# Kernel tuning notes

Measured on AMD Instinct MI355X. Metric: run time of the kernel, lower is better.

## Reference

```python
import jax, jax.numpy as jnp
import numpy as np

B, N, D, H = 4, 2048, 256, 8
d = D // H          # 32 per-head dim
EPS = 1e-5
SCALE = 1.0 / float(np.sqrt(d))


def setup_inputs() -> dict:
    key = jax.random.key(0)
    ks = jax.random.split(key, 6)
    s = 0.02
    x = jax.random.normal(ks[0], (B, N, D), jnp.float32)
    # RoPE frequencies: theta_j = 10000^(-2j/d), angle = pos * theta
    inv_freq = 1.0 / (10000.0 ** (jnp.arange(0, d, 2, dtype=jnp.float32) / d))  # (d/2,)
    ang = jnp.arange(N, dtype=jnp.float32)[:, None] * inv_freq[None, :]          # (N, d/2)
    return {
        "x": x,
        "freqs_cos": jnp.cos(ang),
        "freqs_sin": jnp.sin(ang),
        "w_qkv": jax.random.normal(ks[1], (D, 3 * D), jnp.float32) * s,
        "b_qkv": jnp.zeros((3 * D,), jnp.float32),
        "w_proj": jax.random.normal(ks[2], (D, D), jnp.float32) * s,
        "b_proj": jnp.zeros((D,), jnp.float32),
        "ln1_g": jnp.ones((D,), jnp.float32),
        "ln1_b": jnp.zeros((D,), jnp.float32),
        "ln2_g": jnp.ones((D,), jnp.float32),
        "ln2_b": jnp.zeros((D,), jnp.float32),
        "w1": jax.random.normal(ks[3], (D, 2 * D), jnp.float32) * s,
        "b1": jnp.zeros((2 * D,), jnp.float32),
        "w2": jax.random.normal(ks[4], (2 * D, D), jnp.float32) * s,
        "b2": jnp.zeros((D,), jnp.float32),
    }


def _layer_norm(x, g, b):
    mu = jnp.mean(x, axis=-1, keepdims=True)
    var = jnp.mean(jnp.square(x - mu), axis=-1, keepdims=True)
    return (x - mu) * jax.lax.rsqrt(var + EPS) * g + b


def _rope(t, cos, sin):
    # t: (B,H,N,d); interleaved (even,odd) pairs viewed as complex, multiplied by e^{i*ang}
    tr = t.reshape(B, H, N, d // 2, 2)
    te, to = tr[..., 0], tr[..., 1]
    c = cos[None, None, :, :]
    s = sin[None, None, :, :]
    oe = te * c - to * s
    oo = te * s + to * c
    return jnp.stack([oe, oo], axis=-1).reshape(B, H, N, d)


def reference(x, freqs_cos, freqs_sin, w_qkv, b_qkv, w_proj, b_proj,
              ln1_g, ln1_b, ln2_g, ln2_b, w1, b1, w2, b2):
    # Pre-LN MHSA with RoPE (dropout = identity at eval)
    h = _layer_norm(x, ln1_g, ln1_b)
    qkv = (h @ w_qkv + b_qkv).reshape(B, N, 3, H, d).transpose(0, 2, 3, 1, 4)  # (B,3,H,N,d)
    q, k, v = qkv[:, 0], qkv[:, 1], qkv[:, 2]
    q = _rope(q, freqs_cos, freqs_sin)
    k = _rope(k, freqs_cos, freqs_sin)
    attn = jax.nn.softmax(jnp.einsum('bhnd,bhmd->bhnm', q, k) * SCALE, axis=-1)
    out = jnp.einsum('bhnm,bhmd->bhnd', attn, v).transpose(0, 2, 1, 3).reshape(B, N, D)
    x = x + (out @ w_proj + b_proj)
    h = _layer_norm(x, ln2_g, ln2_b)
    ffn = jax.nn.relu(h @ w1 + b1) @ w2 + b2
    return x + ffn
```

## Files before the change

### kernel.cpp

```cpp
#include <hip/hip_runtime.h>
#include <hip/hip_bf16.h>
#include <math.h>

#define Bsz 4
#define Nseq 2048
#define Dm 256
#define Hh 8
#define Hd 32
#define EPS_ 1e-5f
#define SCALE_ 0.17677669529663687f

typedef __attribute__((ext_vector_type(8))) short short8;
typedef __attribute__((ext_vector_type(4))) short short4v;
typedef __attribute__((ext_vector_type(4))) float f32x4;

__device__ __forceinline__ void gload16(const void* g, void* l) {
    __builtin_amdgcn_global_load_lds(
        (const __attribute__((address_space(1))) void*)g,
        (__attribute__((address_space(3))) void*)l, 16, 0, 0);
}

__device__ __forceinline__ short8 read8x2(const __hip_bfloat16* p) {
    short4v lo = *(const short4v*)p;
    short4v hi = *(const short4v*)(p + 4);
    return __builtin_shufflevector(lo, hi, 0, 1, 2, 3, 4, 5, 6, 7);
}

__global__ __launch_bounds__(256) void ln_kernel(const float* __restrict__ x,
                                                 const float* __restrict__ g,
                                                 const float* __restrict__ b,
                                                 __hip_bfloat16* __restrict__ out) {
    int row  = blockIdx.x * 4 + (threadIdx.x >> 6);
    int lane = threadIdx.x & 63;
    const float* xr = x + (size_t)row * Dm;
    float4 v = *(const float4*)(xr + lane * 4);
    float s  = v.x + v.y + v.z + v.w;
    float ss = v.x * v.x + v.y * v.y + v.z * v.z + v.w * v.w;
    #pragma unroll
    for (int off = 32; off; off >>= 1) {
        s  += __shfl_xor(s, off);
        ss += __shfl_xor(ss, off);
    }
    float mu  = s * (1.0f / Dm);
    float var = ss * (1.0f / Dm) - mu * mu;
    float rs  = rsqrtf(var + EPS_);
    float4 gv = *(const float4*)(g + lane * 4);
    float4 bv = *(const float4*)(b + lane * 4);
    float o0 = (v.x - mu) * rs * gv.x + bv.x;
    float o1 = (v.y - mu) * rs * gv.y + bv.y;
    float o2 = (v.z - mu) * rs * gv.z + bv.z;
    float o3 = (v.w - mu) * rs * gv.w + bv.w;
    __hip_bfloat16 h0 = __float2bfloat16(o0), h1 = __float2bfloat16(o1);
    __hip_bfloat16 h2 = __float2bfloat16(o2), h3 = __float2bfloat16(o3);
    short4v o4 = { *(short*)&h0, *(short*)&h1, *(short*)&h2, *(short*)&h3 };
    *(short4v*)(out + (size_t)row * Dm + lane * 4) = o4;
}

__global__ __launch_bounds__(256) void wconv_kernel(
    const float* __restrict__ s0, const float* __restrict__ s1,
    const float* __restrict__ s2, const float* __restrict__ s3,
    __hip_bfloat16* __restrict__ d0, __hip_bfloat16* __restrict__ d1,
    __hip_bfloat16* __restrict__ d2, __hip_bfloat16* __restrict__ d3) {
    __shared__ float t[32][33];
    int bid = blockIdx.x;
    const float* src; __hip_bfloat16* dst; int K, N, tb;
    if (bid < 192)      { src = s0; dst = d0; K = 256; N = 768; tb = bid; }
    else if (bid < 256) { src = s1; dst = d1; K = 256; N = 256; tb = bid - 192; }
    else if (bid < 384) { src = s2; dst = d2; K = 256; N = 512; tb = bid - 256; }
    else                { src = s3; dst = d3; K = 512; N = 256; tb = bid - 384; }
    int tn = N >> 5;
    int k0 = (tb / tn) * 32, n0 = (tb % tn) * 32;
    int c = threadIdx.x & 31, r0 = threadIdx.x >> 5;
    #pragma unroll
    for (int i = 0; i < 4; i++) {
        int r = r0 + i * 8;
        t[r][c] = src[(size_t)(k0 + r) * N + n0 + c];
    }
    __syncthreads();
    #pragma unroll
    for (int i = 0; i < 4; i++) {
        int n = r0 + i * 8;
        dst[(size_t)(n0 + n) * K + k0 + c] = __float2bfloat16(t[c][n]);
    }
}

template <int EPI>
__global__ __launch_bounds__(256) void mfma_gemm(const __hip_bfloat16* __restrict__ A,
                                                 const __hip_bfloat16* __restrict__ Wt,
                                                 const float* __restrict__ bias,
                                                 const float* __restrict__ res,
                                                 float* __restrict__ Cf,
                                                 __hip_bfloat16* __restrict__ Cb,
                                                 int M, int Nn, int K) {
    __shared__ __align__(16) __hip_bfloat16 As[128 * 32];
    __shared__ __align__(16) __hip_bfloat16 Bs[64 * 32];
    const int tid = threadIdx.x, w = tid >> 6, lane = tid & 63;
    const int lm = lane & 15, lq = lane >> 4;
    const int bm = blockIdx.y * 128, bn = blockIdx.x * 64;
    f32x4 acc[2][4];
    #pragma unroll
    for (int i = 0; i < 2; i++)
        #pragma unroll
        for (int j = 0; j < 4; j++) acc[i][j] = (f32x4){0.f, 0.f, 0.f, 0.f};

    const int sw = (lq ^ (lm & 3)) * 8;
    for (int k0 = 0; k0 < K; k0 += 32) {
        #pragma unroll
        for (int p = 0; p < 2; p++) {
            int c = p * 256 + w * 64 + lane;
            int r = c >> 2, gk = ((c & 3) ^ (r & 3)) * 8;
            gload16(A + (size_t)(bm + r) * K + k0 + gk, As + (p * 256 + w * 64) * 8);
        }
        {
            int c = w * 64 + lane;
            int r = c >> 2, gk = ((c & 3) ^ (r & 3)) * 8;
            gload16(Wt + (size_t)(bn + r) * K + k0 + gk, Bs + (w * 64) * 8);
        }
        __syncthreads();
        short8 a0 = *(const short8*)&As[(w * 32 + lm) * 32 + sw];
        short8 a1 = *(const short8*)&As[(w * 32 + 16 + lm) * 32 + sw];
        #pragma unroll
        for (int nf = 0; nf < 4; nf++) {
            short8 bfr = *(const short8*)&Bs[(nf * 16 + lm) * 32 + sw];
            acc[0][nf] = __builtin_amdgcn_mfma_f32_16x16x32_bf16(a0, bfr, acc[0][nf], 0, 0, 0);
            acc[1][nf] = __builtin_amdgcn_mfma_f32_16x16x32_bf16(a1, bfr, acc[1][nf], 0, 0, 0);
        }
        __syncthreads();
    }
    #pragma unroll
    for (int nf = 0; nf < 4; nf++) {
        int cg = bn + nf * 16 + lm;
        float bi = bias[cg];
        #pragma unroll
        for (int mf = 0; mf < 2; mf++) {
            #pragma unroll
            for (int r = 0; r < 4; r++) {
                int rg = bm + w * 32 + mf * 16 + lq * 4 + r;
                float v = acc[mf][nf][r] + bi;
                if (EPI == 1) {
                    v = fmaxf(v, 0.f);
                    Cb[(size_t)rg * Nn + cg] = __float2bfloat16(v);
                } else {
                    v += res[(size_t)rg * Nn + cg];
                    Cf[(size_t)rg * Nn + cg] = v;
                }
            }
        }
    }
}

__global__ __launch_bounds__(256) void qkv_mfma(const __hip_bfloat16* __restrict__ A,
                                                const __hip_bfloat16* __restrict__ Wt,
                                                const float* __restrict__ bias,
                                                const float* __restrict__ fcos,
                                                const float* __restrict__ fsin,
                                                __hip_bfloat16* __restrict__ qout,
                                                __hip_bfloat16* __restrict__ kout,
                                                __hip_bfloat16* __restrict__ vout) {
    const int K = 256, Nn = 768;
    __shared__ __align__(16) __hip_bfloat16 As[128 * 32];
    __shared__ __align__(16) __hip_bfloat16 Bs[64 * 32];
    __shared__ __align__(16) float cosS[2048];
    __shared__ __align__(16) float sinS[2048];
    const int tid = threadIdx.x, w = tid >> 6, lane = tid & 63;
    const int lm = lane & 15, lq = lane >> 4;
    const int bm = blockIdx.y * 128, bn = blockIdx.x * 64;
    f32x4 acc[2][4];
    #pragma unroll
    for (int i = 0; i < 2; i++)
        #pragma unroll
        for (int j = 0; j < 4; j++) acc[i][j] = (f32x4){0.f, 0.f, 0.f, 0.f};

    const int sw = (lq ^ (lm & 3)) * 8;
    for (int k0 = 0; k0 < K; k0 += 32) {
        #pragma unroll
        for (int p = 0; p < 2; p++) {
            int c = p * 256 + w * 64 + lane;
            int r = c >> 2, gk = ((c & 3) ^ (r & 3)) * 8;
            gload16(A + (size_t)(bm + r) * K + k0 + gk, As + (p * 256 + w * 64) * 8);
        }
        {
            int c = w * 64 + lane;
            int r = c >> 2, gk = ((c & 3) ^ (r & 3)) * 8;
            gload16(Wt + (size_t)(bn + r) * K + k0 + gk, Bs + (w * 64) * 8);
        }
        __syncthreads();
        short8 a0 = *(const short8*)&As[(w * 32 + lm) * 32 + sw];
        short8 a1 = *(const short8*)&As[(w * 32 + 16 + lm) * 32 + sw];
        #pragma unroll
        for (int nf = 0; nf < 4; nf++) {
            short8 bfr = *(const short8*)&Bs[(nf * 16 + lm) * 32 + sw];
            acc[0][nf] = __builtin_amdgcn_mfma_f32_16x16x32_bf16(a0, bfr, acc[0][nf], 0, 0, 0);
            acc[1][nf] = __builtin_amdgcn_mfma_f32_16x16x32_bf16(a1, bfr, acc[1][nf], 0, 0, 0);
        }
        __syncthreads();
    }
    int n0 = bm & (Nseq - 1);
    *(float4*)&cosS[tid * 8]     = *(const float4*)&fcos[n0 * 16 + tid * 8];
    *(float4*)&cosS[tid * 8 + 4] = *(const float4*)&fcos[n0 * 16 + tid * 8 + 4];
    *(float4*)&sinS[tid * 8]     = *(const float4*)&fsin[n0 * 16 + tid * 8];
    *(float4*)&sinS[tid * 8 + 4] = *(const float4*)&fsin[n0 * 16 + tid * 8 + 4];
    __syncthreads();

    const int seg = bn >> 8;
    #pragma unroll
    for (int nf = 0; nf < 4; nf++) {
        int cg = bn + nf * 16 + lm;
        int hh = (cg & 255) >> 5;
        int dd = (nf & 1) * 16 + lm;
        int i0 = dd >> 1;
        float bi = bias[cg];
        #pragma unroll
        for (int mf = 0; mf < 2; mf++) {
            #pragma unroll
            for (int r = 0; r < 4; r++) {
                int rg = bm + w * 32 + mf * 16 + lq * 4 + r;
                int nl = rg - bm;
                float v = acc[mf][nf][r] + bi;
                float vp = __shfl_xor(v, 1);
                float outv;
                if (seg < 2) {
                    float cs = cosS[nl * 16 + i0], sn = sinS[nl * 16 + i0];
                    outv = (dd & 1) ? (vp * sn + v * cs) : (v * cs - vp * sn);
                    if (seg == 0) outv *= SCALE_;
                } else {
                    outv = v;
                }
                int bb = rg >> 11, n = rg & (Nseq - 1);
                __hip_bfloat16* dst = (seg == 0) ? qout : ((seg == 1) ? kout : vout);
                dst[(((size_t)(bb * Hh + hh)) * Nseq + n) * Hd + dd] = __float2bfloat16(outv);
            }
        }
    }
}

__global__ __launch_bounds__(256) void attn_mfma(const __hip_bfloat16* __restrict__ q,
                                                 const __hip_bfloat16* __restrict__ k,
                                                 const __hip_bfloat16* __restrict__ v,
                                                 __hip_bfloat16* __restrict__ att) {
    __shared__ __align__(16) __hip_bfloat16 Qs[64 * 32];
    __shared__ __align__(16) __hip_bfloat16 Ks[2][64 * 32];
    __shared__ __align__(16) __hip_bfloat16 Vt[2][32 * 68];
    __shared__ __align__(16) __hip_bfloat16 Ps[4][16 * 68];
    const int tid = threadIdx.x, w = tid >> 6, lane = tid & 63;
    const int lm = lane & 15, lq = lane >> 4;
    const int bh = blockIdx.y, qbase = blockIdx.x * 64;
    const __hip_bfloat16* qp = q + ((size_t)bh * Nseq + qbase) * Hd;
    const __hip_bfloat16* kp = k + (size_t)bh * Nseq * Hd;
    const __hip_bfloat16* vp = v + (size_t)bh * Nseq * Hd;
    const int srow = tid >> 2, sc = tid & 3;
    const int ssw = (sc ^ (srow & 3)) * 8;

    *(float4*)&Qs[srow * 32 + sc * 8] = *(const float4*)(qp + srow * 32 + ssw);
    {
        float4 k4 = *(const float4*)(kp + srow * 32 + ssw);
        float4 v4 = *(const float4*)(vp + (size_t)srow * Hd + sc * 8);
        *(float4*)&Ks[0][srow * 32 + sc * 8] = k4;
        const __hip_bfloat16* vv = (const __hip_bfloat16*)&v4;
        #pragma unroll
        for (int j = 0; j < 8; j++) Vt[0][(sc * 8 + j) * 68 + srow] = vv[j];
    }
    __syncthreads();

    const int sw = (lq ^ (lm & 3)) * 8;
    short8 qf = *(const short8*)&Qs[(w * 16 + lm) * 32 + sw];
    f32x4 O0 = {0.f, 0.f, 0.f, 0.f};
    f32x4 O1 = {0.f, 0.f, 0.f, 0.f};
    float sm[4] = {0.f, 0.f, 0.f, 0.f};

    for (int kt = 0; kt < Nseq / 64; kt++) {
        int cur = kt & 1;
        if (kt + 1 < Nseq / 64) {
            const __hip_bfloat16* kpn = kp + (size_t)(kt + 1) * 64 * Hd;
            float4 k4 = *(const float4*)(kpn + srow * 32 + ssw);
            float4 v4 = *(const float4*)(vp + (size_t)((kt + 1) * 64 + srow) * Hd + sc * 8);
            *(float4*)&Ks[cur ^ 1][srow * 32 + sc * 8] = k4;
            const __hip_bfloat16* vv = (const __hip_bfloat16*)&v4;
            #pragma unroll
            for (int j = 0; j < 8; j++) Vt[cur ^ 1][(sc * 8 + j) * 68 + srow] = vv[j];
        }
        f32x4 S[4];
        #pragma unroll
        for (int kb = 0; kb < 4; kb++) {
            short8 kf = *(const short8*)&Ks[cur][(kb * 16 + lm) * 32 + sw];
            f32x4 zz = {0.f, 0.f, 0.f, 0.f};
            S[kb] = __builtin_amdgcn_mfma_f32_16x16x32_bf16(qf, kf, zz, 0, 0, 0);
        }
        #pragma unroll
        for (int kb = 0; kb < 4; kb++) {
            #pragma unroll
            for (int r = 0; r < 4; r++) {
                float p = __expf(S[kb][r]);
                sm[r] += p;
                Ps[w][(lq * 4 + r) * 68 + kb * 16 + lm] = __float2bfloat16(p);
            }
        }
        #pragma unroll
        for (int sub = 0; sub < 2; sub++) {
            short8 pf  = read8x2(&Ps[w][lm * 68 + sub * 32 + lq * 8]);
            short8 vf0 = read8x2(&Vt[cur][lm * 68 + sub * 32 + lq * 8]);
            short8 vf1 = read8x2(&Vt[cur][(16 + lm) * 68 + sub * 32 + lq * 8]);
            O0 = __builtin_amdgcn_mfma_f32_16x16x32_bf16(pf, vf0, O0, 0, 0, 0);
            O1 = __builtin_amdgcn_mfma_f32_16x16x32_bf16(pf, vf1, O1, 0, 0, 0);
        }
        __syncthreads();
    }
    #pragma unroll
    for (int off = 1; off <= 8; off <<= 1) {
        #pragma unroll
        for (int r = 0; r < 4; r++) sm[r] += __shfl_xor(sm[r], off);
    }
    const int bb = bh >> 3, hh = bh & 7;
    #pragma unroll
    for (int r = 0; r < 4; r++) {
        float inv = 1.0f / sm[r];
        int n = qbase + w * 16 + lq * 4 + r;
        __hip_bfloat16* op = att + ((size_t)(bb * Nseq + n)) * Dm + hh * Hd;
        op[lm]      = __float2bfloat16(O0[r] * inv);
        op[16 + lm] = __float2bfloat16(O1[r] * inv);
    }
}

extern "C" void kernel_launch(void* const* d_in, const int* in_sizes, int n_in,
                              void* d_out, int out_size, void* d_ws, size_t ws_size,
                              hipStream_t stream) {
    const float* x      = (const float*)d_in[0];
    const float* fcos   = (const float*)d_in[1];
    const float* fsin   = (const float*)d_in[2];
    const float* w_qkv  = (const float*)d_in[3];
    const float* b_qkv  = (const float*)d_in[4];
    const float* w_proj = (const float*)d_in[5];
    const float* b_proj = (const float*)d_in[6];
    const float* ln1_g  = (const float*)d_in[7];
    const float* ln1_b  = (const float*)d_in[8];
    const float* ln2_g  = (const float*)d_in[9];
    const float* ln2_b  = (const float*)d_in[10];
    const float* w1     = (const float*)d_in[11];
    const float* b1     = (const float*)d_in[12];
    const float* w2     = (const float*)d_in[13];
    const float* b2     = (const float*)d_in[14];
    float* out = (float*)d_out;
    char* base = (char*)d_ws;
    const size_t MB = (size_t)1 << 20;

    __hip_bfloat16* h   = (__hip_bfloat16*)(base);
    float*          x2f = (float*)(base);
    __hip_bfloat16* qb  = (__hip_bfloat16*)(base + 8 * MB);
    __hip_bfloat16* kbf = (__hip_bfloat16*)(base + 12 * MB);
    __hip_bfloat16* vbf = (__hip_bfloat16*)(base + 16 * MB);
    __hip_bfloat16* att = (__hip_bfloat16*)(base + 20 * MB);
    __hip_bfloat16* h2  = (__hip_bfloat16*)(base + 8 * MB);
    __hip_bfloat16* ffn = (__hip_bfloat16*)(base + 24 * MB);
    __hip_bfloat16* wqT = (__hip_bfloat16*)(base + 32 * MB);
    __hip_bfloat16* wpT = (__hip_bfloat16*)(base + 32 * MB + 393216);
    __hip_bfloat16* w1T = (__hip_bfloat16*)(base + 32 * MB + 524288);
    __hip_bfloat16* w2T = (__hip_bfloat16*)(base + 32 * MB + 786432);

    const int rows = Bsz * Nseq;

    wconv_kernel<<<512, 256, 0, stream>>>(w_qkv, w_proj, w1, w2, wqT, wpT, w1T, w2T);
    ln_kernel<<<rows / 4, 256, 0, stream>>>(x, ln1_g, ln1_b, h);
    qkv_mfma<<<dim3(12, 64), 256, 0, stream>>>(h, wqT, b_qkv, fcos, fsin, qb, kbf, vbf);
    attn_mfma<<<dim3(Nseq / 64, Bsz * Hh), 256, 0, stream>>>(qb, kbf, vbf, att);
    mfma_gemm<2><<<dim3(4, 64), 256, 0, stream>>>(att, wpT, b_proj, x, x2f, nullptr,
                                                  rows, 256, 256);
    ln_kernel<<<rows / 4, 256, 0, stream>>>(x2f, ln2_g, ln2_b, h2);
    mfma_gemm<1><<<dim3(8, 64), 256, 0, stream>>>(h2, w1T, b1, nullptr, nullptr, ffn,
                                                  rows, 512, 256);
    mfma_gemm<2><<<dim3(4, 64), 256, 0, stream>>>(ffn, w2T, b2, x2f, out, nullptr,
                                                  rows, 256, 512);
}
```

Baseline: 192.6 us.

## Rewrite attention with 32x32 MFMA, register-resident P, transposed V from QKV epilogue

The attention kernel now uses 32x32x16 MFMAs computing S^T so the probabilities stay in registers and are repacked across lane halves with shuffles, instead of round-tripping through shared memory. K and V tiles are loaded with async global-to-LDS loads, and V is written pre-transposed by the QKV epilogue. The log2e factor is folded into the Q scale so exp2 replaces exp. The projection and FFN2 GEMMs switch to 64-row tiles for more blocks, and the QKV epilogue reads cos/sin directly from global memory instead of staging them in LDS. Softmax stays without max subtraction, as before, which relies on small logits.

```diff
diff --git a/kernel.cpp b/kernel.cpp
--- a/kernel.cpp
+++ b/kernel.cpp
@@ -9,10 +9,12 @@
 #define Hd 32
 #define EPS_ 1e-5f
 #define SCALE_ 0.17677669529663687f
+#define QSC_ (0.17677669529663687f * 1.4426950408889634f)
 
 typedef __attribute__((ext_vector_type(8))) short short8;
 typedef __attribute__((ext_vector_type(4))) short short4v;
 typedef __attribute__((ext_vector_type(4))) float f32x4;
+typedef __attribute__((ext_vector_type(16))) float f32x16;
 
 __device__ __forceinline__ void gload16(const void* g, void* l) {
     __builtin_amdgcn_global_load_lds(
@@ -20,11 +22,18 @@
         (__attribute__((address_space(3))) void*)l, 16, 0, 0);
 }
 
-__device__ __forceinline__ short8 read8x2(const __hip_bfloat16* p) {
-    short4v lo = *(const short4v*)p;
-    short4v hi = *(const short4v*)(p + 4);
-    return __builtin_shufflevector(lo, hi, 0, 1, 2, 3, 4, 5, 6, 7);
-}
+__device__ __forceinline__ short bf16s(float f) {
+    __hip_bfloat16 h = __float2bfloat16(f);
+    return *(short*)&h;
+}
+
+__device__ __forceinline__ int pkbf(float a, float b) {
+    __hip_bfloat16 lo = __float2bfloat16(a), hi2 = __float2bfloat16(b);
+    return (int)(((unsigned int)*(unsigned short*)&hi2 << 16) |
+                 (unsigned int)*(unsigned short*)&lo);
+}
+
+union I4S8 { int i[4]; short8 s; };
 
 __global__ __launch_bounds__(256) void ln_kernel(const float* __restrict__ x,
                                                  const float* __restrict__ g,
@@ -46,13 +55,10 @@
     float rs  = rsqrtf(var + EPS_);
     float4 gv = *(const float4*)(g + lane * 4);
     float4 bv = *(const float4*)(b + lane * 4);
-    float o0 = (v.x - mu) * rs * gv.x + bv.x;
-    float o1 = (v.y - mu) * rs * gv.y + bv.y;
-    float o2 = (v.z - mu) * rs * gv.z + bv.z;
-    float o3 = (v.w - mu) * rs * gv.w + bv.w;
-    __hip_bfloat16 h0 = __float2bfloat16(o0), h1 = __float2bfloat16(o1);
-    __hip_bfloat16 h2 = __float2bfloat16(o2), h3 = __float2bfloat16(o3);
-    short4v o4 = { *(short*)&h0, *(short*)&h1, *(short*)&h2, *(short*)&h3 };
+    short4v o4 = { bf16s((v.x - mu) * rs * gv.x + bv.x),
+                   bf16s((v.y - mu) * rs * gv.y + bv.y),
+                   bf16s((v.z - mu) * rs * gv.z + bv.z),
+                   bf16s((v.w - mu) * rs * gv.w + bv.w) };
     *(short4v*)(out + (size_t)row * Dm + lane * 4) = o4;
 }
 
@@ -84,7 +90,7 @@
     }
 }
 
-template <int EPI>
+template <int TM, int EPI>
 __global__ __launch_bounds__(256) void mfma_gemm(const __hip_bfloat16* __restrict__ A,
                                                  const __hip_bfloat16* __restrict__ Wt,
                                                  const float* __restrict__ bias,
@@ -92,38 +98,41 @@
                                                  float* __restrict__ Cf,
                                                  __hip_bfloat16* __restrict__ Cb,
                                                  int M, int Nn, int K) {
-    __shared__ __align__(16) __hip_bfloat16 As[128 * 32];
+    constexpr int MF = TM / 64;
+    __shared__ __align__(16) __hip_bfloat16 As[TM * 32];
     __shared__ __align__(16) __hip_bfloat16 Bs[64 * 32];
     const int tid = threadIdx.x, w = tid >> 6, lane = tid & 63;
     const int lm = lane & 15, lq = lane >> 4;
-    const int bm = blockIdx.y * 128, bn = blockIdx.x * 64;
-    f32x4 acc[2][4];
-    #pragma unroll
-    for (int i = 0; i < 2; i++)
+    const int bm = blockIdx.y * TM, bn = blockIdx.x * 64;
+    f32x4 acc[MF][4];
+    #pragma unroll
+    for (int i = 0; i < MF; i++)
         #pragma unroll
         for (int j = 0; j < 4; j++) acc[i][j] = (f32x4){0.f, 0.f, 0.f, 0.f};
 
     const int sw = (lq ^ (lm & 3)) * 8;
     for (int k0 = 0; k0 < K; k0 += 32) {
         #pragma unroll
-        for (int p = 0; p < 2; p++) {
-            int c = p * 256 + w * 64 + lane;
+        for (int p = 0; p < MF; p++) {
+            int c = p * 256 + tid;
             int r = c >> 2, gk = ((c & 3) ^ (r & 3)) * 8;
             gload16(A + (size_t)(bm + r) * K + k0 + gk, As + (p * 256 + w * 64) * 8);
         }
         {
-            int c = w * 64 + lane;
-            int r = c >> 2, gk = ((c & 3) ^ (r & 3)) * 8;
-            gload16(Wt + (size_t)(bn + r) * K + k0 + gk, Bs + (w * 64) * 8);
-        }
-        __syncthreads();
-        short8 a0 = *(const short8*)&As[(w * 32 + lm) * 32 + sw];
-        short8 a1 = *(const short8*)&As[(w * 32 + 16 + lm) * 32 + sw];
+            int r = tid >> 2, gk = ((tid & 3) ^ (r & 3)) * 8;
+            gload16(Wt + (size_t)(bn + r) * K + k0 + gk, Bs + w * 512);
+        }
+        __syncthreads();
+        short8 a[MF];
+        #pragma unroll
+        for (int mf = 0; mf < MF; mf++)
+            a[mf] = *(const short8*)&As[(w * (TM / 4) + mf * 16 + lm) * 32 + sw];
         #pragma unroll
         for (int nf = 0; nf < 4; nf++) {
             short8 bfr = *(const short8*)&Bs[(nf * 16 + lm) * 32 + sw];
-            acc[0][nf] = __builtin_amdgcn_mfma_f32_16x16x32_bf16(a0, bfr, acc[0][nf], 0, 0, 0);
-            acc[1][nf] = __builtin_amdgcn_mfma_f32_16x16x32_bf16(a1, bfr, acc[1][nf], 0, 0, 0);
+            #pragma unroll
+            for (int mf = 0; mf < MF; mf++)
+                acc[mf][nf] = __builtin_amdgcn_mfma_f32_16x16x32_bf16(a[mf], bfr, acc[mf][nf], 0, 0, 0);
         }
         __syncthreads();
     }
@@ -132,10 +141,10 @@
         int cg = bn + nf * 16 + lm;
         float bi = bias[cg];
         #pragma unroll
-        for (int mf = 0; mf < 2; mf++) {
+        for (int mf = 0; mf < MF; mf++) {
             #pragma unroll
             for (int r = 0; r < 4; r++) {
-                int rg = bm + w * 32 + mf * 16 + lq * 4 + r;
+                int rg = bm + w * (TM / 4) + mf * 16 + lq * 4 + r;
                 float v = acc[mf][nf][r] + bi;
                 if (EPI == 1) {
                     v = fmaxf(v, 0.f);
@@ -156,12 +165,10 @@
                                                 const float* __restrict__ fsin,
                                                 __hip_bfloat16* __restrict__ qout,
                                                 __hip_bfloat16* __restrict__ kout,
-                                                __hip_bfloat16* __restrict__ vout) {
+                                                __hip_bfloat16* __restrict__ vt) {
     const int K = 256, Nn = 768;
     __shared__ __align__(16) __hip_bfloat16 As[128 * 32];
     __shared__ __align__(16) __hip_bfloat16 Bs[64 * 32];
-    __shared__ __align__(16) float cosS[2048];
-    __shared__ __align__(16) float sinS[2048];
     const int tid = threadIdx.x, w = tid >> 6, lane = tid & 63;
     const int lm = lane & 15, lq = lane >> 4;
     const int bm = blockIdx.y * 128, bn = blockIdx.x * 64;
@@ -175,14 +182,13 @@
     for (int k0 = 0; k0 < K; k0 += 32) {
         #pragma unroll
         for (int p = 0; p < 2; p++) {
-            int c = p * 256 + w * 64 + lane;
+            int c = p * 256 + tid;
             int r = c >> 2, gk = ((c & 3) ^ (r & 3)) * 8;
             gload16(A + (size_t)(bm + r) * K + k0 + gk, As + (p * 256 + w * 64) * 8);
         }
         {
-            int c = w * 64 + lane;
-            int r = c >> 2, gk = ((c & 3) ^ (r & 3)) * 8;
-            gload16(Wt + (size_t)(bn + r) * K + k0 + gk, Bs + (w * 64) * 8);
+            int r = tid >> 2, gk = ((tid & 3) ^ (r & 3)) * 8;
+            gload16(Wt + (size_t)(bn + r) * K + k0 + gk, Bs + w * 512);
         }
         __syncthreads();
         short8 a0 = *(const short8*)&As[(w * 32 + lm) * 32 + sw];
@@ -195,13 +201,6 @@
         }
         __syncthreads();
     }
-    int n0 = bm & (Nseq - 1);
-    *(float4*)&cosS[tid * 8]     = *(const float4*)&fcos[n0 * 16 + tid * 8];
-    *(float4*)&cosS[tid * 8 + 4] = *(const float4*)&fcos[n0 * 16 + tid * 8 + 4];
-    *(float4*)&sinS[tid * 8]     = *(const float4*)&fsin[n0 * 16 + tid * 8];
-    *(float4*)&sinS[tid * 8 + 4] = *(const float4*)&fsin[n0 * 16 + tid * 8 + 4];
-    __syncthreads();
-
     const int seg = bn >> 8;
     #pragma unroll
     for (int nf = 0; nf < 4; nf++) {
@@ -215,20 +214,18 @@
             #pragma unroll
             for (int r = 0; r < 4; r++) {
                 int rg = bm + w * 32 + mf * 16 + lq * 4 + r;
-                int nl = rg - bm;
+                int bb = rg >> 11, n = rg & (Nseq - 1);
                 float v = acc[mf][nf][r] + bi;
-                float vp = __shfl_xor(v, 1);
-                float outv;
-                if (seg < 2) {
-                    float cs = cosS[nl * 16 + i0], sn = sinS[nl * 16 + i0];
-                    outv = (dd & 1) ? (vp * sn + v * cs) : (v * cs - vp * sn);
-                    if (seg == 0) outv *= SCALE_;
+                if (seg == 2) {
+                    vt[(((size_t)(bb * Hh + hh)) * Hd + dd) * Nseq + n] = __float2bfloat16(v);
                 } else {
-                    outv = v;
+                    float vp = __shfl_xor(v, 1);
+                    float cs = fcos[n * 16 + i0], sn = fsin[n * 16 + i0];
+                    float outv = (dd & 1) ? (vp * sn + v * cs) : (v * cs - vp * sn);
+                    if (seg == 0) outv *= QSC_;
+                    __hip_bfloat16* dst = (seg == 0) ? qout : kout;
+                    dst[(((size_t)(bb * Hh + hh)) * Nseq + n) * Hd + dd] = __float2bfloat16(outv);
                 }
-                int bb = rg >> 11, n = rg & (Nseq - 1);
-                __hip_bfloat16* dst = (seg == 0) ? qout : ((seg == 1) ? kout : vout);
-                dst[(((size_t)(bb * Hh + hh)) * Nseq + n) * Hd + dd] = __float2bfloat16(outv);
             }
         }
     }
@@ -236,88 +233,111 @@
 
 __global__ __launch_bounds__(256) void attn_mfma(const __hip_bfloat16* __restrict__ q,
                                                  const __hip_bfloat16* __restrict__ k,
-                                                 const __hip_bfloat16* __restrict__ v,
+                                                 const __hip_bfloat16* __restrict__ vt,
                                                  __hip_bfloat16* __restrict__ att) {
-    __shared__ __align__(16) __hip_bfloat16 Qs[64 * 32];
-    __shared__ __align__(16) __hip_bfloat16 Ks[2][64 * 32];
-    __shared__ __align__(16) __hip_bfloat16 Vt[2][32 * 68];
-    __shared__ __align__(16) __hip_bfloat16 Ps[4][16 * 68];
-    const int tid = threadIdx.x, w = tid >> 6, lane = tid & 63;
-    const int lm = lane & 15, lq = lane >> 4;
-    const int bh = blockIdx.y, qbase = blockIdx.x * 64;
+    __shared__ __align__(16) __hip_bfloat16 Qs[128 * 32];
+    __shared__ __align__(16) __hip_bfloat16 Ks[2][32 * 64];
+    __shared__ __align__(16) __hip_bfloat16 Vs[2][32 * 64];
+    __shared__ float smS[4][32];
+    const int tid = threadIdx.x, w = tid >> 6;
+    const int lane = tid & 63, l31 = lane & 31, hi = lane >> 5;
+    const int bh = blockIdx.y, qbase = blockIdx.x * 128;
     const __hip_bfloat16* qp = q + ((size_t)bh * Nseq + qbase) * Hd;
     const __hip_bfloat16* kp = k + (size_t)bh * Nseq * Hd;
-    const __hip_bfloat16* vp = v + (size_t)bh * Nseq * Hd;
-    const int srow = tid >> 2, sc = tid & 3;
-    const int ssw = (sc ^ (srow & 3)) * 8;
-
-    *(float4*)&Qs[srow * 32 + sc * 8] = *(const float4*)(qp + srow * 32 + ssw);
-    {
-        float4 k4 = *(const float4*)(kp + srow * 32 + ssw);
-        float4 v4 = *(const float4*)(vp + (size_t)srow * Hd + sc * 8);
-        *(float4*)&Ks[0][srow * 32 + sc * 8] = k4;
-        const __hip_bfloat16* vv = (const __hip_bfloat16*)&v4;
-        #pragma unroll
-        for (int j = 0; j < 8; j++) Vt[0][(sc * 8 + j) * 68 + srow] = vv[j];
-    }
+    const __hip_bfloat16* vp = vt + (size_t)bh * Hd * Nseq;
+
+    const int r8 = tid >> 3, s8 = tid & 7;
+    #pragma unroll
+    for (int p = 0; p < 2; p++) {
+        int c = p * 256 + tid, r = c >> 2, sl = c & 3;
+        gload16(qp + r * 32 + ((sl ^ (r & 3)) * 8), Qs + (p * 256 + w * 64) * 8);
+    }
+    gload16(kp + (2 * r8 + (s8 >> 2)) * 32 + (((s8 & 3) ^ (r8 & 3)) * 8), Ks[0] + w * 512);
+    gload16(vp + (size_t)r8 * Nseq + ((s8 ^ (r8 & 7)) * 8), Vs[0] + w * 512);
     __syncthreads();
 
-    const int sw = (lq ^ (lm & 3)) * 8;
-    short8 qf = *(const short8*)&Qs[(w * 16 + lm) * 32 + sw];
-    f32x4 O0 = {0.f, 0.f, 0.f, 0.f};
-    f32x4 O1 = {0.f, 0.f, 0.f, 0.f};
-    float sm[4] = {0.f, 0.f, 0.f, 0.f};
+    const int qrow = w * 32 + l31;
+    short8 qf0 = *(const short8*)&Qs[qrow * 32 + ((hi ^ (l31 & 3)) * 8)];
+    short8 qf1 = *(const short8*)&Qs[qrow * 32 + (((2 + hi) ^ (l31 & 3)) * 8)];
+
+    f32x16 O;
+    #pragma unroll
+    for (int i = 0; i < 16; i++) O[i] = 0.f;
+    float sm = 0.f;
 
     for (int kt = 0; kt < Nseq / 64; kt++) {
-        int cur = kt & 1;
+        const int cur = kt & 1;
         if (kt + 1 < Nseq / 64) {
-            const __hip_bfloat16* kpn = kp + (size_t)(kt + 1) * 64 * Hd;
-            float4 k4 = *(const float4*)(kpn + srow * 32 + ssw);
-            float4 v4 = *(const float4*)(vp + (size_t)((kt + 1) * 64 + srow) * Hd + sc * 8);
-            *(float4*)&Ks[cur ^ 1][srow * 32 + sc * 8] = k4;
-            const __hip_bfloat16* vv = (const __hip_bfloat16*)&v4;
-            #pragma unroll
-            for (int j = 0; j < 8; j++) Vt[cur ^ 1][(sc * 8 + j) * 68 + srow] = vv[j];
-        }
-        f32x4 S[4];
-        #pragma unroll
-        for (int kb = 0; kb < 4; kb++) {
-            short8 kf = *(const short8*)&Ks[cur][(kb * 16 + lm) * 32 + sw];
-            f32x4 zz = {0.f, 0.f, 0.f, 0.f};
-            S[kb] = __builtin_amdgcn_mfma_f32_16x16x32_bf16(qf, kf, zz, 0, 0, 0);
-        }
-        #pragma unroll
-        for (int kb = 0; kb < 4; kb++) {
-            #pragma unroll
-            for (int r = 0; r < 4; r++) {
-                float p = __expf(S[kb][r]);
-                sm[r] += p;
-                Ps[w][(lq * 4 + r) * 68 + kb * 16 + lm] = __float2bfloat16(p);
-            }
-        }
-        #pragma unroll
-        for (int sub = 0; sub < 2; sub++) {
-            short8 pf  = read8x2(&Ps[w][lm * 68 + sub * 32 + lq * 8]);
-            short8 vf0 = read8x2(&Vt[cur][lm * 68 + sub * 32 + lq * 8]);
-            short8 vf1 = read8x2(&Vt[cur][(16 + lm) * 68 + sub * 32 + lq * 8]);
-            O0 = __builtin_amdgcn_mfma_f32_16x16x32_bf16(pf, vf0, O0, 0, 0, 0);
-            O1 = __builtin_amdgcn_mfma_f32_16x16x32_bf16(pf, vf1, O1, 0, 0, 0);
-        }
-        __syncthreads();
-    }
-    #pragma unroll
-    for (int off = 1; off <= 8; off <<= 1) {
-        #pragma unroll
-        for (int r = 0; r < 4; r++) sm[r] += __shfl_xor(sm[r], off);
-    }
+            gload16(kp + ((kt + 1) * 64 + 2 * r8 + (s8 >> 2)) * 32 + (((s8 & 3) ^ (r8 & 3)) * 8),
+                    Ks[cur ^ 1] + w * 512);
+            gload16(vp + (size_t)r8 * Nseq + (kt + 1) * 64 + ((s8 ^ (r8 & 7)) * 8),
+                    Vs[cur ^ 1] + w * 512);
+        }
+        f32x16 St0, St1;
+        #pragma unroll
+        for (int i = 0; i < 16; i++) { St0[i] = 0.f; St1[i] = 0.f; }
+        {
+            int prow = l31 >> 1;
+            int elb = prow * 64 + (l31 & 1) * 32;
+            short8 kf0 = *(const short8*)&Ks[cur][elb + ((hi ^ (prow & 3)) * 8)];
+            short8 kf1 = *(const short8*)&Ks[cur][elb + (((2 + hi) ^ (prow & 3)) * 8)];
+            St0 = __builtin_amdgcn_mfma_f32_32x32x16_bf16(kf0, qf0, St0, 0, 0, 0);
+            St0 = __builtin_amdgcn_mfma_f32_32x32x16_bf16(kf1, qf1, St0, 0, 0, 0);
+        }
+        {
+            int prow = 16 + (l31 >> 1);
+            int elb = prow * 64 + (l31 & 1) * 32;
+            short8 kf0 = *(const short8*)&Ks[cur][elb + ((hi ^ (prow & 3)) * 8)];
+            short8 kf1 = *(const short8*)&Ks[cur][elb + (((2 + hi) ^ (prow & 3)) * 8)];
+            St1 = __builtin_amdgcn_mfma_f32_32x32x16_bf16(kf0, qf0, St1, 0, 0, 0);
+            St1 = __builtin_amdgcn_mfma_f32_32x32x16_bf16(kf1, qf1, St1, 0, 0, 0);
+        }
+        int pk0[8], pk1[8];
+        #pragma unroll
+        for (int p = 0; p < 8; p++) {
+            float a = exp2f(St0[2 * p]), b = exp2f(St0[2 * p + 1]);
+            sm += a + b;
+            pk0[p] = pkbf(a, b);
+        }
+        #pragma unroll
+        for (int p = 0; p < 8; p++) {
+            float a = exp2f(St1[2 * p]), b = exp2f(St1[2 * p + 1]);
+            sm += a + b;
+            pk1[p] = pkbf(a, b);
+        }
+        #pragma unroll
+        for (int t = 0; t < 4; t++) {
+            const int* PK = (t >> 1) ? pk1 : pk0;
+            const int base = 4 * (t & 1);
+            int keep0 = hi ? PK[base + 2] : PK[base + 0];
+            int keep1 = hi ? PK[base + 3] : PK[base + 1];
+            int send0 = hi ? PK[base + 0] : PK[base + 2];
+            int send1 = hi ? PK[base + 1] : PK[base + 3];
+            int x0 = __shfl_xor(send0, 32);
+            int x1 = __shfl_xor(send1, 32);
+            I4S8 u;
+            u.i[0] = hi ? x0 : keep0;
+            u.i[1] = hi ? x1 : keep1;
+            u.i[2] = hi ? keep0 : x0;
+            u.i[3] = hi ? keep1 : x1;
+            short8 vf = *(const short8*)&Vs[cur][l31 * 64 + (((2 * t + hi) ^ (l31 & 7)) * 8)];
+            O = __builtin_amdgcn_mfma_f32_32x32x16_bf16(u.s, vf, O, 0, 0, 0);
+        }
+        __syncthreads();
+    }
+    sm += __shfl_xor(sm, 32);
+    if (hi == 0) smS[w][l31] = sm;
+    __syncthreads();
     const int bb = bh >> 3, hh = bh & 7;
     #pragma unroll
-    for (int r = 0; r < 4; r++) {
-        float inv = 1.0f / sm[r];
-        int n = qbase + w * 16 + lq * 4 + r;
-        __hip_bfloat16* op = att + ((size_t)(bb * Nseq + n)) * Dm + hh * Hd;
-        op[lm]      = __float2bfloat16(O0[r] * inv);
-        op[16 + lm] = __float2bfloat16(O1[r] * inv);
+    for (int m = 0; m < 4; m++) {
+        float4 sv = *(const float4*)&smS[w][8 * m + 4 * hi];
+        #pragma unroll
+        for (int i = 0; i < 4; i++) {
+            int n = qbase + w * 32 + 8 * m + 4 * hi + i;
+            att[((size_t)(bb * Nseq + n)) * Dm + hh * Hd + l31] =
+                __float2bfloat16(O[4 * m + i] * (1.0f / sv[i]));
+        }
     }
 }
 
@@ -344,29 +364,29 @@
     const size_t MB = (size_t)1 << 20;
 
     __hip_bfloat16* h   = (__hip_bfloat16*)(base);
-    float*          x2f = (float*)(base);
-    __hip_bfloat16* qb  = (__hip_bfloat16*)(base + 8 * MB);
-    __hip_bfloat16* kbf = (__hip_bfloat16*)(base + 12 * MB);
-    __hip_bfloat16* vbf = (__hip_bfloat16*)(base + 16 * MB);
-    __hip_bfloat16* att = (__hip_bfloat16*)(base + 20 * MB);
-    __hip_bfloat16* h2  = (__hip_bfloat16*)(base + 8 * MB);
-    __hip_bfloat16* ffn = (__hip_bfloat16*)(base + 24 * MB);
-    __hip_bfloat16* wqT = (__hip_bfloat16*)(base + 32 * MB);
-    __hip_bfloat16* wpT = (__hip_bfloat16*)(base + 32 * MB + 393216);
-    __hip_bfloat16* w1T = (__hip_bfloat16*)(base + 32 * MB + 524288);
-    __hip_bfloat16* w2T = (__hip_bfloat16*)(base + 32 * MB + 786432);
+    __hip_bfloat16* qb  = (__hip_bfloat16*)(base + 4 * MB);
+    __hip_bfloat16* kbf = (__hip_bfloat16*)(base + 8 * MB);
+    __hip_bfloat16* vtb = (__hip_bfloat16*)(base + 12 * MB);
+    __hip_bfloat16* att = (__hip_bfloat16*)(base + 16 * MB);
+    float*          x2f = (float*)(base + 20 * MB);
+    __hip_bfloat16* h2  = (__hip_bfloat16*)(base);
+    __hip_bfloat16* ffn = (__hip_bfloat16*)(base + 28 * MB);
+    __hip_bfloat16* wqT = (__hip_bfloat16*)(base + 40 * MB);
+    __hip_bfloat16* wpT = (__hip_bfloat16*)(base + 40 * MB + 393216);
+    __hip_bfloat16* w1T = (__hip_bfloat16*)(base + 40 * MB + 524288);
+    __hip_bfloat16* w2T = (__hip_bfloat16*)(base + 40 * MB + 786432);
 
     const int rows = Bsz * Nseq;
 
     wconv_kernel<<<512, 256, 0, stream>>>(w_qkv, w_proj, w1, w2, wqT, wpT, w1T, w2T);
     ln_kernel<<<rows / 4, 256, 0, stream>>>(x, ln1_g, ln1_b, h);
-    qkv_mfma<<<dim3(12, 64), 256, 0, stream>>>(h, wqT, b_qkv, fcos, fsin, qb, kbf, vbf);
-    attn_mfma<<<dim3(Nseq / 64, Bsz * Hh), 256, 0, stream>>>(qb, kbf, vbf, att);
-    mfma_gemm<2><<<dim3(4, 64), 256, 0, stream>>>(att, wpT, b_proj, x, x2f, nullptr,
-                                                  rows, 256, 256);
+    qkv_mfma<<<dim3(12, 64), 256, 0, stream>>>(h, wqT, b_qkv, fcos, fsin, qb, kbf, vtb);
+    attn_mfma<<<dim3(Nseq / 128, Bsz * Hh), 256, 0, stream>>>(qb, kbf, vtb, att);
+    mfma_gemm<64, 2><<<dim3(4, 128), 256, 0, stream>>>(att, wpT, b_proj, x, x2f, nullptr,
+                                                       rows, 256, 256);
     ln_kernel<<<rows / 4, 256, 0, stream>>>(x2f, ln2_g, ln2_b, h2);
-    mfma_gemm<1><<<dim3(8, 64), 256, 0, stream>>>(h2, w1T, b1, nullptr, nullptr, ffn,
-                                                  rows, 512, 256);
-    mfma_gemm<2><<<dim3(4, 64), 256, 0, stream>>>(ffn, w2T, b2, x2f, out, nullptr,
-                                                  rows, 256, 512);
-}
+    mfma_gemm<128, 1><<<dim3(8, 64), 256, 0, stream>>>(h2, w1T, b1, nullptr, nullptr, ffn,
+                                                       rows, 512, 256);
+    mfma_gemm<64, 2><<<dim3(4, 128), 256, 0, stream>>>(ffn, w2T, b2, x2f, out, nullptr,
+                                                       rows, 256, 512);
+}
```

After: 205.0 us. 6.5% more time.
